# Performance work log

Hardware: AMD Instinct MI355X
Metric: run time of the kernel (lower is better)

Reference implementation:

```python
import jax, jax.numpy as jnp
import numpy as np

N = 50000       # nodes
E = 800000      # edges
IN, H, OUT = 256, 512, 64


def gcn_conv(x, src, dst, norm, W, b, n_nodes):
    # PyG GCNConv: linear transform first, then normalized scatter-add aggregation.
    xw = x @ W                                   # [N, H]
    msg = xw[src] * norm[:, None]                # [E+N, H] gathered, normalized messages
    out = jax.ops.segment_sum(msg, dst, num_segments=n_nodes)
    return out + b


def setup_inputs() -> dict:
    key = jax.random.key(0)
    ks = jax.random.split(key, 8)
    x = jax.random.normal(ks[0], (N, IN), dtype=jnp.float32)
    edge_index = jax.random.randint(ks[1], (2, E), 0, N, dtype=jnp.int64)
    W1 = jax.random.normal(ks[2], (IN, H), dtype=jnp.float32) * (1.0 / np.sqrt(IN))
    b1 = jnp.zeros((H,), dtype=jnp.float32)
    W2 = jax.random.normal(ks[3], (H, H), dtype=jnp.float32) * (1.0 / np.sqrt(H))
    b2 = jnp.zeros((H,), dtype=jnp.float32)
    Wl = jax.random.normal(ks[4], (H, OUT), dtype=jnp.float32) * (1.0 / np.sqrt(H))
    bl = jnp.zeros((OUT,), dtype=jnp.float32)
    return {"x": x, "edge_index": edge_index, "W1": W1, "b1": b1,
            "W2": W2, "b2": b2, "Wl": Wl, "bl": bl}


def reference(x, edge_index, W1, b1, W2, b2, Wl, bl):
    n = x.shape[0]
    loop = jnp.arange(n, dtype=edge_index.dtype)
    src = jnp.concatenate([edge_index[0], loop])     # add self-loops
    dst = jnp.concatenate([edge_index[1], loop])
    # symmetric normalization D^-1/2 (A+I) D^-1/2
    deg = jax.ops.segment_sum(jnp.ones_like(dst, dtype=x.dtype), dst, num_segments=n)
    dinv = jnp.where(deg > 0, jax.lax.rsqrt(jnp.maximum(deg, 1.0)), 0.0)
    norm = dinv[src] * dinv[dst]                      # [E+N]

    h = jax.nn.relu(gcn_conv(x, src, dst, norm, W1, b1, n))
    # dropout omitted (deterministic eval reference)
    h = jax.nn.relu(gcn_conv(h, src, dst, norm, W2, b2, n))
    return h @ Wl + bl
```

## Files before the change

kernel.cpp:

```cpp
#include <hip/hip_runtime.h>
#include <cstdint>
#include <cstddef>

typedef unsigned short u16;
typedef __attribute__((ext_vector_type(8))) _Float16 f16x8;
typedef __attribute__((ext_vector_type(4))) float f32x4;
typedef __attribute__((ext_vector_type(2))) unsigned u32x2;
typedef __attribute__((ext_vector_type(4))) unsigned u32x4;

__device__ __forceinline__ u16 f2h(float f) {
    union { _Float16 h; u16 u; } v; v.h = (_Float16)f;
    return v.u;
}
__device__ __forceinline__ float h2f(u16 b) {
    union { u16 u; _Float16 h; } v; v.u = b;
    return (float)v.h;
}
__device__ __forceinline__ float h2f_lo(unsigned w) { return h2f((u16)(w & 0xFFFFu)); }
__device__ __forceinline__ float h2f_hi(unsigned w) { return h2f((u16)(w >> 16)); }

__device__ __forceinline__ void gload16(const u16* g, u16* l) {
    __builtin_amdgcn_global_load_lds(
        (const __attribute__((address_space(1))) void*)g,
        (__attribute__((address_space(3))) void*)l, 16, 0, 0);
}

__global__ void init_deg_kernel(float* __restrict__ deg, int n) {
    int i = blockIdx.x * blockDim.x + threadIdx.x;
    if (i < n) deg[i] = 1.0f;
}

__global__ void count_deg_kernel(const int* __restrict__ dst, float* __restrict__ deg, int e) {
    int i = blockIdx.x * blockDim.x + threadIdx.x;
    if (i < e) atomicAdd(&deg[dst[i]], 1.0f);
}

__global__ __launch_bounds__(1024)
void scan1_kernel(const float* __restrict__ deg, int* __restrict__ part, int n) {
    __shared__ int sm[1024];
    const int t = threadIdx.x;
    const int i = blockIdx.x * 1024 + t;
    sm[t] = (i < n) ? (int)deg[i] - 1 : 0;
    __syncthreads();
    for (int off = 512; off > 0; off >>= 1) {
        if (t < off) sm[t] += sm[t + off];
        __syncthreads();
    }
    if (t == 0) part[blockIdx.x] = sm[0];
}

__global__ __launch_bounds__(1024)
void scan2_kernel(int* __restrict__ part, int nb) {
    __shared__ int sm[1024];
    const int t = threadIdx.x;
    const int v = (t < nb) ? part[t] : 0;
    sm[t] = v;
    __syncthreads();
    for (int off = 1; off < 1024; off <<= 1) {
        int tv = (t >= off) ? sm[t - off] : 0;
        __syncthreads();
        sm[t] += tv;
        __syncthreads();
    }
    if (t < nb) part[t] = sm[t] - v;
}

__global__ __launch_bounds__(1024)
void scan3_kernel(const float* __restrict__ deg, const int* __restrict__ part,
                  float* __restrict__ dinv, int* __restrict__ row_start,
                  int* __restrict__ cursor, int n) {
    __shared__ int sm[1024];
    const int t = threadIdx.x;
    const int b = blockIdx.x;
    const int i = b * 1024 + t;
    int v = 0;
    float d = 1.f;
    if (i < n) {
        d = deg[i];
        v = (int)d - 1;
    }
    sm[t] = v;
    __syncthreads();
    for (int off = 1; off < 1024; off <<= 1) {
        int tv = (t >= off) ? sm[t - off] : 0;
        __syncthreads();
        sm[t] += tv;
        __syncthreads();
    }
    if (i < n) {
        row_start[i] = part[b] + sm[t] - v;
        dinv[i] = rsqrtf(d);
        cursor[i] = 0;
    }
    if (i == n - 1) row_start[n] = part[b] + sm[t];
}

__global__ void bucket_kernel(const int* __restrict__ src, const int* __restrict__ dst,
                              const int* __restrict__ row_start, int* __restrict__ cursor,
                              int* __restrict__ csr, float* __restrict__ csr_w,
                              const float* __restrict__ dinv, int e) {
    int i = blockIdx.x * blockDim.x + threadIdx.x;
    if (i < e) {
        int d = dst[i];
        int s = src[i];
        int pos = atomicAdd(&cursor[d], 1);
        int at = row_start[d] + pos;
        csr[at] = s;
        csr_w[at] = dinv[s] * dinv[d];
    }
}

__global__ void wtrans_kernel(const float* __restrict__ W, u16* __restrict__ bt, int K, int N) {
    const int k8 = K >> 3;
    const int idx = blockIdx.x * blockDim.x + threadIdx.x;
    if (idx >= N * k8) return;
    const int n = idx / k8;
    const int k0 = (idx - n * k8) * 8;
    alignas(16) u16 h8[8];
#pragma unroll
    for (int j = 0; j < 8; j++) h8[j] = f2h(W[(size_t)(k0 + j) * N + n]);
    *(uint4*)(bt + (size_t)n * K + k0) = *(const uint4*)h8;
}

__global__ void xsplit_kernel(const float* __restrict__ x, u16* __restrict__ xh, size_t total8) {
    const size_t idx = (size_t)blockIdx.x * blockDim.x + threadIdx.x;
    if (idx >= total8) return;
    const float4 v0 = *(const float4*)(x + idx * 8);
    const float4 v1 = *(const float4*)(x + idx * 8 + 4);
    alignas(16) u16 h8[8];
    h8[0] = f2h(v0.x); h8[1] = f2h(v0.y); h8[2] = f2h(v0.z); h8[3] = f2h(v0.w);
    h8[4] = f2h(v1.x); h8[5] = f2h(v1.y); h8[6] = f2h(v1.z); h8[7] = f2h(v1.w);
    *(uint4*)(xh + idx * 8) = *(const uint4*)h8;
}

__global__ __launch_bounds__(256)
void agg_x_kernel(const float* __restrict__ x, const u16* __restrict__ xh,
                  u16* __restrict__ oh,
                  const int* __restrict__ csr, const float* __restrict__ csr_w,
                  const int* __restrict__ rs, const float* __restrict__ dinv, int n) {
    const int node = blockIdx.x * 4 + (threadIdx.x >> 6);
    if (node >= n) return;
    const int lane = threadIdx.x & 63;
    const int c0 = lane * 4;
    const int beg = rs[node], end = rs[node + 1];
    float a0 = 0.f, a1 = 0.f, a2 = 0.f, a3 = 0.f;
    int i = beg;
    for (; i + 8 <= end; i += 8) {
        int s[8];
        float w[8];
        uint2 hv[8];
#pragma unroll
        for (int u = 0; u < 8; u++) {
            s[u] = __builtin_nontemporal_load(csr + i + u);
            w[u] = __builtin_nontemporal_load(csr_w + i + u);
        }
#pragma unroll
        for (int u = 0; u < 8; u++) hv[u] = *(const uint2*)(xh + (size_t)s[u] * 256 + c0);
#pragma unroll
        for (int u = 0; u < 8; u++) {
            a0 = fmaf(h2f_lo(hv[u].x), w[u], a0);
            a1 = fmaf(h2f_hi(hv[u].x), w[u], a1);
            a2 = fmaf(h2f_lo(hv[u].y), w[u], a2);
            a3 = fmaf(h2f_hi(hv[u].y), w[u], a3);
        }
    }
    for (; i < end; i++) {
        const int sv = csr[i];
        const float w = csr_w[i];
        uint2 hv = *(const uint2*)(xh + (size_t)sv * 256 + c0);
        a0 = fmaf(h2f_lo(hv.x), w, a0);
        a1 = fmaf(h2f_hi(hv.x), w, a1);
        a2 = fmaf(h2f_lo(hv.y), w, a2);
        a3 = fmaf(h2f_hi(hv.y), w, a3);
    }
    {
        const float dn = dinv[node];
        const float ws = dn * dn;
        const float4 xv = *(const float4*)(x + (size_t)node * 256 + c0);
        a0 = fmaf(xv.x, ws, a0);
        a1 = fmaf(xv.y, ws, a1);
        a2 = fmaf(xv.z, ws, a2);
        a3 = fmaf(xv.w, ws, a3);
    }
    u32x2 ho;
    ho.x = (unsigned)f2h(a0) | ((unsigned)f2h(a1) << 16);
    ho.y = (unsigned)f2h(a2) | ((unsigned)f2h(a3) << 16);
    __builtin_nontemporal_store(ho, (u32x2*)(oh + (size_t)node * 256 + c0));
}

__global__ __launch_bounds__(256)
void agg_h_kernel(const u16* __restrict__ hin, u16* __restrict__ oh,
                  const int* __restrict__ csr, const float* __restrict__ csr_w,
                  const int* __restrict__ rs, const float* __restrict__ dinv, int n) {
    const int node = blockIdx.x * 4 + (threadIdx.x >> 6);
    if (node >= n) return;
    const int lane = threadIdx.x & 63;
    const int c0 = lane * 8;
    const int beg = rs[node], end = rs[node + 1];
    float a[8];
#pragma unroll
    for (int j = 0; j < 8; j++) a[j] = 0.f;
    int i = beg;
    for (; i + 4 <= end; i += 4) {
        int s[4];
        float w[4];
        uint4 hv[4];
#pragma unroll
        for (int u = 0; u < 4; u++) {
            s[u] = __builtin_nontemporal_load(csr + i + u);
            w[u] = __builtin_nontemporal_load(csr_w + i + u);
        }
#pragma unroll
        for (int u = 0; u < 4; u++) hv[u] = *(const uint4*)(hin + (size_t)s[u] * 512 + c0);
#pragma unroll
        for (int u = 0; u < 4; u++) {
            a[0] = fmaf(h2f_lo(hv[u].x), w[u], a[0]);
            a[1] = fmaf(h2f_hi(hv[u].x), w[u], a[1]);
            a[2] = fmaf(h2f_lo(hv[u].y), w[u], a[2]);
            a[3] = fmaf(h2f_hi(hv[u].y), w[u], a[3]);
            a[4] = fmaf(h2f_lo(hv[u].z), w[u], a[4]);
            a[5] = fmaf(h2f_hi(hv[u].z), w[u], a[5]);
            a[6] = fmaf(h2f_lo(hv[u].w), w[u], a[6]);
            a[7] = fmaf(h2f_hi(hv[u].w), w[u], a[7]);
        }
    }
    for (; i < end; i++) {
        const int sv = csr[i];
        const float w = csr_w[i];
        uint4 hv = *(const uint4*)(hin + (size_t)sv * 512 + c0);
        a[0] = fmaf(h2f_lo(hv.x), w, a[0]);
        a[1] = fmaf(h2f_hi(hv.x), w, a[1]);
        a[2] = fmaf(h2f_lo(hv.y), w, a[2]);
        a[3] = fmaf(h2f_hi(hv.y), w, a[3]);
        a[4] = fmaf(h2f_lo(hv.z), w, a[4]);
        a[5] = fmaf(h2f_hi(hv.z), w, a[5]);
        a[6] = fmaf(h2f_lo(hv.w), w, a[6]);
        a[7] = fmaf(h2f_hi(hv.w), w, a[7]);
    }
    {
        const float dn = dinv[node];
        const float ws = dn * dn;
        uint4 hv = *(const uint4*)(hin + (size_t)node * 512 + c0);
        a[0] = fmaf(h2f_lo(hv.x), ws, a[0]);
        a[1] = fmaf(h2f_hi(hv.x), ws, a[1]);
        a[2] = fmaf(h2f_lo(hv.y), ws, a[2]);
        a[3] = fmaf(h2f_hi(hv.y), ws, a[3]);
        a[4] = fmaf(h2f_lo(hv.z), ws, a[4]);
        a[5] = fmaf(h2f_hi(hv.z), ws, a[5]);
        a[6] = fmaf(h2f_lo(hv.w), ws, a[6]);
        a[7] = fmaf(h2f_hi(hv.w), ws, a[7]);
    }
    u32x4 ho;
#pragma unroll
    for (int j = 0; j < 4; j++)
        ho[j] = (unsigned)f2h(a[2 * j]) | ((unsigned)f2h(a[2 * j + 1]) << 16);
    __builtin_nontemporal_store(ho, (u32x4*)(oh + (size_t)node * 512 + c0));
}

template <bool RELU, int OUTMODE>
__global__ __launch_bounds__(512)
void gemm256_kernel(const u16* __restrict__ A, const u16* __restrict__ Bt,
                    const float* __restrict__ bias,
                    float* __restrict__ Cf, u16* __restrict__ Ch,
                    int M, int K, int Nn) {
    __shared__ u16 sA[2][128 * 32], sB[2][256 * 32];

    const int gx = gridDim.x;
    const int nwg = gx * gridDim.y;
    const int orig = blockIdx.y * gx + blockIdx.x;
    const int q8 = nwg >> 3, r8 = nwg & 7;
    const int xcd = orig & 7, lin = orig >> 3;
    const int wg = (xcd < r8 ? xcd * (q8 + 1) : r8 * (q8 + 1) + (xcd - r8) * q8) + lin;
    const int mt = wg / gx;
    const int nt_ = wg - mt * gx;
    const int m0 = mt * 128, n0 = nt_ * 256;

    const int tid = threadIdx.x;
    const int lane = tid & 63;
    const int wid = tid >> 6;
    const int wm = (wid >> 2) * 64;
    const int wn = (wid & 3) * 64;

    const int srow = tid >> 2;
    const int gslot = (tid & 3) ^ ((tid >> 3) & 3);
    const int lbase = wid * 16 * 32;

    const u16* gA  = A  + (size_t)(m0 + srow) * K + gslot * 8;
    const u16* gB0 = Bt + (size_t)(n0 + srow) * K + gslot * 8;
    const u16* gB1 = Bt + (size_t)(n0 + 128 + srow) * K + gslot * 8;

    int offA[4], offB[4];
    const int q = lane >> 4;
#pragma unroll
    for (int i = 0; i < 4; i++) {
        int r = wm + i * 16 + (lane & 15);
        offA[i] = r * 32 + ((q ^ ((r >> 1) & 3)) * 8);
    }
#pragma unroll
    for (int j = 0; j < 4; j++) {
        int r = wn + j * 16 + (lane & 15);
        offB[j] = r * 32 + ((q ^ ((r >> 1) & 3)) * 8);
    }

    f32x4 acc[4][4];
#pragma unroll
    for (int i = 0; i < 4; i++)
#pragma unroll
        for (int j = 0; j < 4; j++) acc[i][j] = (f32x4){0.f, 0.f, 0.f, 0.f};

    auto stage = [&](int k0, int b) {
        gload16(gA + k0, sA[b] + lbase);
        gload16(gB0 + k0, sB[b] + lbase);
        gload16(gB1 + k0, sB[b] + 128 * 32 + lbase);
    };

    const int ntiles = K >> 5;
    stage(0, 0);
    for (int t = 0; t < ntiles; ++t) {
        const int cur = t & 1;
        __builtin_amdgcn_s_barrier();
        if (t + 1 < ntiles) {
            stage((t + 1) << 5, cur ^ 1);
            asm volatile("s_waitcnt vmcnt(3)" ::: "memory");
        } else {
            asm volatile("s_waitcnt vmcnt(0)" ::: "memory");
        }
        __builtin_amdgcn_s_barrier();
        __builtin_amdgcn_sched_barrier(0);

        f16x8 af[4], bf4[4];
#pragma unroll
        for (int i = 0; i < 4; i++) af[i] = *(const f16x8*)(sA[cur] + offA[i]);
#pragma unroll
        for (int j = 0; j < 4; j++) bf4[j] = *(const f16x8*)(sB[cur] + offB[j]);
#pragma unroll
        for (int i = 0; i < 4; i++)
#pragma unroll
            for (int j = 0; j < 4; j++)
                acc[i][j] = __builtin_amdgcn_mfma_f32_16x16x32_f16(af[i], bf4[j], acc[i][j], 0, 0, 0);
    }

    const int cn = lane & 15;
    const int cm = (lane >> 4) * 4;
#pragma unroll
    for (int i = 0; i < 4; i++) {
#pragma unroll
        for (int j = 0; j < 4; j++) {
            const int col = n0 + wn + j * 16 + cn;
            const float bv = bias[col];
#pragma unroll
            for (int r = 0; r < 4; r++) {
                const int row = m0 + wm + i * 16 + cm + r;
                if (row < M) {
                    float v = acc[i][j][r] + bv;
                    if (RELU) v = fmaxf(v, 0.f);
                    if constexpr (OUTMODE == 2) {
                        Ch[(size_t)row * Nn + col] = f2h(v);
                    } else {
                        Cf[(size_t)row * Nn + col] = v;
                    }
                }
            }
        }
    }
}

template <bool RELU>
__global__ __launch_bounds__(256)
void gemm64_kernel(const u16* __restrict__ A, const u16* __restrict__ Bt,
                   const float* __restrict__ bias, float* __restrict__ Cf,
                   int M, int K, int Nn) {
    __shared__ u16 sA[128 * 32], sB[64 * 32];

    const int nwg = gridDim.y;
    const int orig = blockIdx.y;
    const int q8 = nwg >> 3, r8 = nwg & 7;
    const int xcd = orig & 7, lin = orig >> 3;
    const int wg = (xcd < r8 ? xcd * (q8 + 1) : r8 * (q8 + 1) + (xcd - r8) * q8) + lin;
    const int m0 = wg * 128, n0 = 0;

    const int tid = threadIdx.x;
    const int lane = tid & 63;
    const int wid = tid >> 6;
    const int wm = (wid >> 1) * 64;
    const int wn = (wid & 1) * 32;

    const int srow = tid >> 2;
    const int gslot = (tid & 3) ^ ((tid >> 3) & 3);
    const int lbase = wid * 16 * 32;

    const u16* gA0 = A + (size_t)(m0 + srow) * K + gslot * 8;
    const u16* gA1 = A + (size_t)(m0 + 64 + srow) * K + gslot * 8;
    const u16* gB0 = Bt + (size_t)(n0 + srow) * K + gslot * 8;

    int offA[4], offB[2];
    const int q = lane >> 4;
#pragma unroll
    for (int i = 0; i < 4; i++) {
        int r = wm + i * 16 + (lane & 15);
        offA[i] = r * 32 + ((q ^ ((r >> 1) & 3)) * 8);
    }
#pragma unroll
    for (int j = 0; j < 2; j++) {
        int r = wn + j * 16 + (lane & 15);
        offB[j] = r * 32 + ((q ^ ((r >> 1) & 3)) * 8);
    }

    f32x4 acc[4][2];
#pragma unroll
    for (int i = 0; i < 4; i++)
#pragma unroll
        for (int j = 0; j < 2; j++) acc[i][j] = (f32x4){0.f, 0.f, 0.f, 0.f};

    auto stage = [&](int k0) {
        gload16(gA0 + k0, sA + lbase);
        gload16(gA1 + k0, sA + 64 * 32 + lbase);
        gload16(gB0 + k0, sB + lbase);
    };

    stage(0);
    for (int k0 = 0; k0 < K; k0 += 32) {
        __syncthreads();
        f16x8 af[4], bf4[2];
#pragma unroll
        for (int i = 0; i < 4; i++) af[i] = *(const f16x8*)(sA + offA[i]);
#pragma unroll
        for (int j = 0; j < 2; j++) bf4[j] = *(const f16x8*)(sB + offB[j]);
#pragma unroll
        for (int i = 0; i < 4; i++)
#pragma unroll
            for (int j = 0; j < 2; j++)
                acc[i][j] = __builtin_amdgcn_mfma_f32_16x16x32_f16(af[i], bf4[j], acc[i][j], 0, 0, 0);
        __syncthreads();
        if (k0 + 32 < K) stage(k0 + 32);
    }

    const int cn = lane & 15;
    const int cm = (lane >> 4) * 4;
#pragma unroll
    for (int i = 0; i < 4; i++) {
#pragma unroll
        for (int j = 0; j < 2; j++) {
            const int col = wn + j * 16 + cn;
            const float bv = bias[col];
#pragma unroll
            for (int r = 0; r < 4; r++) {
                const int row = m0 + wm + i * 16 + cm + r;
                if (row < M) {
                    float v = acc[i][j][r] + bv;
                    if (RELU) v = fmaxf(v, 0.f);
                    Cf[(size_t)row * Nn + col] = v;
                }
            }
        }
    }
}

extern "C" void kernel_launch(void* const* d_in, const int* in_sizes, int n_in,
                              void* d_out, int out_size, void* d_ws, size_t ws_size,
                              hipStream_t stream) {
    const float* x  = (const float*)d_in[0];
    const int*   ei = (const int*)d_in[1];
    const float* W1 = (const float*)d_in[2];
    const float* b1 = (const float*)d_in[3];
    const float* W2 = (const float*)d_in[4];
    const float* b2 = (const float*)d_in[5];
    const float* Wl = (const float*)d_in[6];
    const float* bl = (const float*)d_in[7];
    float* out = (float*)d_out;

    const int N = in_sizes[0] / 256;
    const int E = in_sizes[1] / 2;
    const int Mpad = ((N + 127) / 128) * 128;
    const int nb = (N + 1023) / 1024;
    const int* src = ei;
    const int* dst = ei + E;

    size_t off = 0;
    auto alloc = [&](size_t bytes) -> void* {
        void* p = (char*)d_ws + off;
        off += (bytes + 255) & ~(size_t)255;
        return p;
    };
    float* deg       = (float*)alloc((size_t)N * 4);
    float* dinv      = (float*)alloc((size_t)N * 4);
    int*   part      = (int*)alloc((size_t)1024 * 4);
    int*   row_start = (int*)alloc((size_t)(N + 1) * 4);
    int*   cursor    = (int*)alloc((size_t)N * 4);
    int*   csr       = (int*)alloc((size_t)E * 4);
    float* csr_w     = (float*)alloc((size_t)E * 4);
    u16*   xh        = (u16*)alloc((size_t)N * 256 * 2);
    u16*   bt1 = (u16*)alloc((size_t)512 * 256 * 2);
    u16*   bt2 = (u16*)alloc((size_t)512 * 512 * 2);
    u16*   bt3 = (u16*)alloc((size_t)64 * 512 * 2);
    u16*   slabA = (u16*)alloc((size_t)Mpad * 512 * 2);
    u16*   slabH = (u16*)alloc((size_t)Mpad * 512 * 2);
    (void)ws_size;

    u16* a1h = slabA;
    u16* a2h = slabA;
    u16* h1h = slabH;
    u16* h2h = slabH;

    init_deg_kernel<<<(N + 255) / 256, 256, 0, stream>>>(deg, N);
    count_deg_kernel<<<(E + 255) / 256, 256, 0, stream>>>(dst, deg, E);
    scan1_kernel<<<nb, 1024, 0, stream>>>(deg, part, N);
    scan2_kernel<<<1, 1024, 0, stream>>>(part, nb);
    scan3_kernel<<<nb, 1024, 0, stream>>>(deg, part, dinv, row_start, cursor, N);
    bucket_kernel<<<(E + 255) / 256, 256, 0, stream>>>(src, dst, row_start, cursor, csr, csr_w, dinv, E);

    wtrans_kernel<<<(512 * 32 + 255) / 256, 256, 0, stream>>>(W1, bt1, 256, 512);
    wtrans_kernel<<<(512 * 64 + 255) / 256, 256, 0, stream>>>(W2, bt2, 512, 512);
    wtrans_kernel<<<(64 * 64 + 255) / 256, 256, 0, stream>>>(Wl, bt3, 512, 64);
    xsplit_kernel<<<((N * 32) + 255) / 256, 256, 0, stream>>>(x, xh, (size_t)N * 32);

    agg_x_kernel<<<(N + 3) / 4, 256, 0, stream>>>(x, xh, a1h, csr, csr_w, row_start, dinv, N);
    gemm256_kernel<true, 2><<<dim3(2, Mpad / 128), 512, 0, stream>>>(
        a1h, bt1, b1, nullptr, h1h, N, 256, 512);

    agg_h_kernel<<<(N + 3) / 4, 256, 0, stream>>>(h1h, a2h, csr, csr_w, row_start, dinv, N);
    gemm256_kernel<true, 2><<<dim3(2, Mpad / 128), 512, 0, stream>>>(
        a2h, bt2, b2, nullptr, h2h, N, 512, 512);

    gemm64_kernel<false><<<dim3(1, Mpad / 128), 256, 0, stream>>>(
        h2h, bt3, bl, out, N, 512, 64);
}
```

Baseline: 444.3 us.

## Use int degree counts, merge weight transposes, unroll layer-2 aggregation deeper

Degree counting now uses integer atomics into a memset-zeroed buffer, which removes the init kernel and the float conversions. The three weight-transpose launches are merged into one kernel. The first aggregation reads the self-loop term from the fp16 copy instead of the fp32 input, and the second aggregation unrolls its gather loop from 4 to 8 neighbours to keep more loads in flight. Together these cut launch count and memory traffic, at the cost of more registers in the unrolled loop and a slight precision change on the self term.

```diff
diff --git a/kernel.cpp b/kernel.cpp
--- a/kernel.cpp
+++ b/kernel.cpp
@@ -25,22 +25,17 @@
         (__attribute__((address_space(3))) void*)l, 16, 0, 0);
 }
 
-__global__ void init_deg_kernel(float* __restrict__ deg, int n) {
+__global__ void count_deg_kernel(const int* __restrict__ dst, int* __restrict__ deg, int e) {
     int i = blockIdx.x * blockDim.x + threadIdx.x;
-    if (i < n) deg[i] = 1.0f;
-}
-
-__global__ void count_deg_kernel(const int* __restrict__ dst, float* __restrict__ deg, int e) {
-    int i = blockIdx.x * blockDim.x + threadIdx.x;
-    if (i < e) atomicAdd(&deg[dst[i]], 1.0f);
+    if (i < e) atomicAdd(&deg[dst[i]], 1);
 }
 
 __global__ __launch_bounds__(1024)
-void scan1_kernel(const float* __restrict__ deg, int* __restrict__ part, int n) {
+void scan1_kernel(const int* __restrict__ deg, int* __restrict__ part, int n) {
     __shared__ int sm[1024];
     const int t = threadIdx.x;
     const int i = blockIdx.x * 1024 + t;
-    sm[t] = (i < n) ? (int)deg[i] - 1 : 0;
+    sm[t] = (i < n) ? deg[i] : 0;
     __syncthreads();
     for (int off = 512; off > 0; off >>= 1) {
         if (t < off) sm[t] += sm[t + off];
@@ -66,7 +61,7 @@
 }
 
 __global__ __launch_bounds__(1024)
-void scan3_kernel(const float* __restrict__ deg, const int* __restrict__ part,
+void scan3_kernel(const int* __restrict__ deg, const int* __restrict__ part,
                   float* __restrict__ dinv, int* __restrict__ row_start,
                   int* __restrict__ cursor, int n) {
     __shared__ int sm[1024];
@@ -74,11 +69,7 @@
     const int b = blockIdx.x;
     const int i = b * 1024 + t;
     int v = 0;
-    float d = 1.f;
-    if (i < n) {
-        d = deg[i];
-        v = (int)d - 1;
-    }
+    if (i < n) v = deg[i];
     sm[t] = v;
     __syncthreads();
     for (int off = 1; off < 1024; off <<= 1) {
@@ -89,7 +80,7 @@
     }
     if (i < n) {
         row_start[i] = part[b] + sm[t] - v;
-        dinv[i] = rsqrtf(d);
+        dinv[i] = rsqrtf(1.0f + (float)v);
         cursor[i] = 0;
     }
     if (i == n - 1) row_start[n] = part[b] + sm[t];
@@ -110,10 +101,25 @@
     }
 }
 
-__global__ void wtrans_kernel(const float* __restrict__ W, u16* __restrict__ bt, int K, int N) {
+__global__ void wtrans_all_kernel(const float* __restrict__ W1, const float* __restrict__ W2,
+                                  const float* __restrict__ Wl, u16* __restrict__ bt1,
+                                  u16* __restrict__ bt2, u16* __restrict__ bt3) {
+    int idx = blockIdx.x * blockDim.x + threadIdx.x;
+    const float* W;
+    u16* bt;
+    int K, N;
+    if (idx < 16384) {
+        W = W1; bt = bt1; K = 256; N = 512;
+    } else if (idx < 16384 + 32768) {
+        idx -= 16384;
+        W = W2; bt = bt2; K = 512; N = 512;
+    } else if (idx < 16384 + 32768 + 4096) {
+        idx -= 16384 + 32768;
+        W = Wl; bt = bt3; K = 512; N = 64;
+    } else {
+        return;
+    }
     const int k8 = K >> 3;
-    const int idx = blockIdx.x * blockDim.x + threadIdx.x;
-    if (idx >= N * k8) return;
     const int n = idx / k8;
     const int k0 = (idx - n * k8) * 8;
     alignas(16) u16 h8[8];
@@ -134,8 +140,7 @@
 }
 
 __global__ __launch_bounds__(256)
-void agg_x_kernel(const float* __restrict__ x, const u16* __restrict__ xh,
-                  u16* __restrict__ oh,
+void agg_x_kernel(const u16* __restrict__ xh, u16* __restrict__ oh,
                   const int* __restrict__ csr, const float* __restrict__ csr_w,
                   const int* __restrict__ rs, const float* __restrict__ dinv, int n) {
     const int node = blockIdx.x * 4 + (threadIdx.x >> 6);
@@ -176,11 +181,11 @@
     {
         const float dn = dinv[node];
         const float ws = dn * dn;
-        const float4 xv = *(const float4*)(x + (size_t)node * 256 + c0);
-        a0 = fmaf(xv.x, ws, a0);
-        a1 = fmaf(xv.y, ws, a1);
-        a2 = fmaf(xv.z, ws, a2);
-        a3 = fmaf(xv.w, ws, a3);
+        uint2 hv = *(const uint2*)(xh + (size_t)node * 256 + c0);
+        a0 = fmaf(h2f_lo(hv.x), ws, a0);
+        a1 = fmaf(h2f_hi(hv.x), ws, a1);
+        a2 = fmaf(h2f_lo(hv.y), ws, a2);
+        a3 = fmaf(h2f_hi(hv.y), ws, a3);
     }
     u32x2 ho;
     ho.x = (unsigned)f2h(a0) | ((unsigned)f2h(a1) << 16);
@@ -201,19 +206,19 @@
 #pragma unroll
     for (int j = 0; j < 8; j++) a[j] = 0.f;
     int i = beg;
-    for (; i + 4 <= end; i += 4) {
-        int s[4];
-        float w[4];
-        uint4 hv[4];
-#pragma unroll
-        for (int u = 0; u < 4; u++) {
+    for (; i + 8 <= end; i += 8) {
+        int s[8];
+        float w[8];
+        uint4 hv[8];
+#pragma unroll
+        for (int u = 0; u < 8; u++) {
             s[u] = __builtin_nontemporal_load(csr + i + u);
             w[u] = __builtin_nontemporal_load(csr_w + i + u);
         }
 #pragma unroll
-        for (int u = 0; u < 4; u++) hv[u] = *(const uint4*)(hin + (size_t)s[u] * 512 + c0);
-#pragma unroll
-        for (int u = 0; u < 4; u++) {
+        for (int u = 0; u < 8; u++) hv[u] = *(const uint4*)(hin + (size_t)s[u] * 512 + c0);
+#pragma unroll
+        for (int u = 0; u < 8; u++) {
             a[0] = fmaf(h2f_lo(hv[u].x), w[u], a[0]);
             a[1] = fmaf(h2f_hi(hv[u].x), w[u], a[1]);
             a[2] = fmaf(h2f_lo(hv[u].y), w[u], a[2]);
@@ -482,7 +487,7 @@
         off += (bytes + 255) & ~(size_t)255;
         return p;
     };
-    float* deg       = (float*)alloc((size_t)N * 4);
+    int*   deg       = (int*)alloc((size_t)N * 4);
     float* dinv      = (float*)alloc((size_t)N * 4);
     int*   part      = (int*)alloc((size_t)1024 * 4);
     int*   row_start = (int*)alloc((size_t)(N + 1) * 4);
@@ -502,19 +507,18 @@
     u16* h1h = slabH;
     u16* h2h = slabH;
 
-    init_deg_kernel<<<(N + 255) / 256, 256, 0, stream>>>(deg, N);
+    hipMemsetAsync(deg, 0, (size_t)N * 4, stream);
     count_deg_kernel<<<(E + 255) / 256, 256, 0, stream>>>(dst, deg, E);
     scan1_kernel<<<nb, 1024, 0, stream>>>(deg, part, N);
     scan2_kernel<<<1, 1024, 0, stream>>>(part, nb);
     scan3_kernel<<<nb, 1024, 0, stream>>>(deg, part, dinv, row_start, cursor, N);
     bucket_kernel<<<(E + 255) / 256, 256, 0, stream>>>(src, dst, row_start, cursor, csr, csr_w, dinv, E);
 
-    wtrans_kernel<<<(512 * 32 + 255) / 256, 256, 0, stream>>>(W1, bt1, 256, 512);
-    wtrans_kernel<<<(512 * 64 + 255) / 256, 256, 0, stream>>>(W2, bt2, 512, 512);
-    wtrans_kernel<<<(64 * 64 + 255) / 256, 256, 0, stream>>>(Wl, bt3, 512, 64);
+    wtrans_all_kernel<<<(16384 + 32768 + 4096 + 255) / 256, 256, 0, stream>>>(
+        W1, W2, Wl, bt1, bt2, bt3);
     xsplit_kernel<<<((N * 32) + 255) / 256, 256, 0, stream>>>(x, xh, (size_t)N * 32);
 
-    agg_x_kernel<<<(N + 3) / 4, 256, 0, stream>>>(x, xh, a1h, csr, csr_w, row_start, dinv, N);
+    agg_x_kernel<<<(N + 3) / 4, 256, 0, stream>>>(xh, a1h, csr, csr_w, row_start, dinv, N);
     gemm256_kernel<true, 2><<<dim3(2, Mpad / 128), 512, 0, stream>>>(
         a1h, bt1, b1, nullptr, h1h, N, 256, 512);
 
```

Measured after the change: 417.0 us. 1.07x faster.
